# Kernel optimization log

Measured on AMD Instinct MI355X. Metric: run time of the kernel, lower is better.

## Reference

```python
import jax, jax.numpy as jnp
import numpy as np

WIN = 7
K1, K2 = 0.01, 0.03
NP_ = WIN * WIN
COV_NORM = NP_ / (NP_ - 1)


def _box_conv(x, w):
    return jax.lax.conv_general_dilated(
        x, w, window_strides=(1, 1), padding='VALID',
        dimension_numbers=('NCHW', 'OIHW', 'NCHW'))


def setup_inputs() -> dict:
    key = jax.random.key(0)
    k1, k2 = jax.random.split(key)
    B, C, H, W = 64, 2, 320, 320
    X = jax.random.uniform(k1, (B, C, H, W), dtype=jnp.float32)
    Y = jax.random.uniform(k2, (B, C, H, W), dtype=jnp.float32)
    data_range = jnp.ones((B, 1, 1, 1), dtype=jnp.float32)
    w = jnp.ones((1, C, WIN, WIN), dtype=jnp.float32) / (WIN * WIN)
    return {"X": X, "Y": Y, "data_range": data_range, "w": w}


def reference(X, Y, data_range, w):
    C1 = (K1 * data_range) ** 2
    C2 = (K2 * data_range) ** 2
    ux = _box_conv(X, w)
    uy = _box_conv(Y, w)
    uxx = _box_conv(X * X, w)
    uyy = _box_conv(Y * Y, w)
    uxy = _box_conv(X * Y, w)
    vx = COV_NORM * (uxx - ux * ux)
    vy = COV_NORM * (uyy - uy * uy)
    vxy = COV_NORM * (uxy - ux * uy)
    A1 = 2 * ux * uy + C1
    A2 = 2 * vxy + C2
    B1 = ux ** 2 + uy ** 2 + C1
    B2 = vx + vy + C2
    S = (A1 * A2) / (B1 * B2)
    return 1 - S.mean()
```

## Files before the change

kernel.cpp:

```cpp
#include <hip/hip_runtime.h>

#define WW 320
#define OWID 314
#define OHEI 314
#define BB 64
#define CW 58
#define NCW 6
#define BROWS 40
#define NBAND 8
#define BPB 2
#define WPB (NCW * BPB)
#define NTH (WPB * 64)
#define NBLK (BB * NBAND / BPB)

#define LOADR(K_)                                                             \
  {                                                                           \
    const int rr  = min(r0 + g7 + (K_), WW - 1);      \
    const int off = rr * WW;                         \
    gx0[K_] = X0[off]; gx1[K_] = X1[off];                                     \
    gy0[K_] = Y0[off]; gy1[K_] = Y1[off];                                     \
  }

#define BODY(K_)                                                              \
  {                                                                           \
    const float x0 = gx0[K_], x1 = gx1[K_];                                   \
    const float y0 = gy0[K_], y1 = gy1[K_];                                   \
    const float px  = x0 + x1;                                                \
    const float py  = y0 + y1;                                                \
    const float p2  = x0 * x0 + x1 * x1 + y0 * y0 + y1 * y1;                  \
    const float pxy = x0 * y0 + x1 * y1;                                      \
    V0 += px  - ring[K_][0]; ring[K_][0] = px;                                \
    V1 += py  - ring[K_][1]; ring[K_][1] = py;                                \
    V2 += p2  - ring[K_][2]; ring[K_][2] = p2;                                \
    V3 += pxy - ring[K_][3]; ring[K_][3] = pxy;                               \
    const int i_ = g7 + (K_);                                                 \
    const int t  = r0 + i_ - 6;                               \
    if (i_ >= 6 && t < tmax) {                         \
      float b0 = V0 + __shfl_down(V0, 1, 64);                                 \
      float b1 = V1 + __shfl_down(V1, 1, 64);                                 \
      float b2 = V2 + __shfl_down(V2, 1, 64);                                 \
      float b3 = V3 + __shfl_down(V3, 1, 64);                                 \
      float q0 = b0 + __shfl_down(b0, 2, 64);                                 \
      float q1 = b1 + __shfl_down(b1, 2, 64);                                 \
      float q2 = b2 + __shfl_down(b2, 2, 64);                                 \
      float q3 = b3 + __shfl_down(b3, 2, 64);                                 \
      float H0 = q0 + __shfl_down(b0, 4, 64) + __shfl_down(V0, 6, 64);        \
      float H1 = q1 + __shfl_down(b1, 4, 64) + __shfl_down(V1, 6, 64);        \
      float H2 = q2 + __shfl_down(b2, 4, 64) + __shfl_down(V2, 6, 64);        \
      float H3 = q3 + __shfl_down(b3, 4, 64) + __shfl_down(V3, 6, 64);        \
      const float ux  = H0 * inv, uy = H1 * inv;                              \
      const float u2  = H2 * inv, uxy = H3 * inv;                             \
      const float vxy = cn * (uxy - ux * uy);                                 \
      const float v2m = cn * (u2 - ux * ux - uy * uy);           \
      const float A1  = 2.0f * ux * uy + C1;                                  \
      const float A2  = 2.0f * vxy + C2;                                      \
      const float B1  = ux * ux + uy * uy + C1;                               \
      const float B2  = v2m + C2;                                             \
      ssum += cmf * (A1 * A2) / (B1 * B2);         \
    }                                                                         \
  }

__global__ __launch_bounds__(NTH, 1) void ssim_main(
    const float* __restrict__ X, const float* __restrict__ Y,
    const float* __restrict__ dr, double* __restrict__ acc,
    unsigned* __restrict__ counter, float* __restrict__ out)
{
    const int w    = threadIdx.x >> 6;
    const int lane = threadIdx.x & 63;
    const int b    = blockIdx.x >> 2;
    const int pair = blockIdx.x & 3;
    const int band = pair * BPB + (w / NCW);
    const int r0   = band * BROWS;
    const int tmax = min(r0 + BROWS, OHEI);

    int c = (w % NCW) * CW + lane;
    const float cmf = (lane < CW && c < OWID) ? 1.0f : 0.0f;
    if (c > WW - 1) c = WW - 1;

    const size_t plane = (size_t)WW * WW;
    const float* X0 = X + (size_t)b * 2 * plane + c;
    const float* X1 = X0 + plane;
    const float* Y0 = Y + (size_t)b * 2 * plane + c;
    const float* Y1 = Y0 + plane;

    const float d  = dr[b];
    const float C1 = (0.01f * d) * (0.01f * d);
    const float C2 = (0.03f * d) * (0.03f * d);
    const float inv = 1.0f / 49.0f;
    const float cn  = 49.0f / 48.0f;

    float ring[7][4];
    #pragma unroll
    for (int k = 0; k < 7; ++k) {
        ring[k][0] = 0.0f; ring[k][1] = 0.0f;
        ring[k][2] = 0.0f; ring[k][3] = 0.0f;
    }
    float V0 = 0.0f, V1 = 0.0f, V2 = 0.0f, V3 = 0.0f;
    float ssum = 0.0f;
    float gx0[7], gx1[7], gy0[7], gy1[7];

    #pragma unroll 1
    for (int g7 = 0; g7 < 49; g7 += 7) {
        LOADR(0) LOADR(1) LOADR(2) LOADR(3) LOADR(4) LOADR(5) LOADR(6)
        BODY(0) BODY(1) BODY(2) BODY(3) BODY(4) BODY(5) BODY(6)
    }

    double local = (double)ssum;
    #pragma unroll
    for (int off = 32; off > 0; off >>= 1)
        local += __shfl_down(local, off, 64);
    __shared__ double wsum[WPB];
    if (lane == 0) wsum[w] = local;
    __syncthreads();
    if (threadIdx.x == 0) {
        double tot = 0.0;
        #pragma unroll
        for (int k = 0; k < WPB; ++k) tot += wsum[k];
        atomicAdd(acc, tot);
        __threadfence();
        unsigned ticket = atomicAdd(counter, 1u);
        if (ticket == NBLK - 1) {
            double stot = atomicAdd(acc, 0.0);
            const double N = (double)BB * (double)OHEI * (double)OWID;
            out[0] = (float)(1.0 - stot / N);
        }
    }
}

extern "C" void kernel_launch(void* const* d_in, const int* in_sizes, int n_in,
                              void* d_out, int out_size, void* d_ws, size_t ws_size,
                              hipStream_t stream)
{
    const float* X  = (const float*)d_in[0];
    const float* Y  = (const float*)d_in[1];
    const float* dr = (const float*)d_in[2];
    double*   acc     = (double*)d_ws;
    unsigned* counter = (unsigned*)((char*)d_ws + 8);
    float*    out     = (float*)d_out;

    hipMemsetAsync(d_ws, 0, 16, stream);
    ssim_main<<<dim3(NBLK), dim3(NTH), 0, stream>>>(X, Y, dr, acc, counter, out);
}
```

Baseline: 136.7 us.

## Process two columns per lane with float2 loads and shorter row bands

Each lane now handles two adjacent output columns, loaded with float2, and shares partial horizontal sums between the even and odd columns through a paired shuffle scheme. That cuts the column overlap between waves from 6 waves of 58 columns to 3 waves of 122 columns. Row bands shrink from 40 to 20, giving 16 bands per image in 4 blocks of 12 waves each. The aim is fewer redundant loads and fewer shuffles per output. The costs are more vertical halo rows per output and more registers for the doubled ring buffer.

```diff
diff --git a/kernel.cpp b/kernel.cpp
--- a/kernel.cpp
+++ b/kernel.cpp
@@ -4,59 +4,81 @@
 #define OWID 314
 #define OHEI 314
 #define BB 64
-#define CW 58
-#define NCW 6
-#define BROWS 40
-#define NBAND 8
-#define BPB 2
-#define WPB (NCW * BPB)
+#define CPW 122
+#define NCW 3
+#define BROWS 20
+#define NBANDB 4
+#define WPB (NCW * NBANDB)
 #define NTH (WPB * 64)
-#define NBLK (BB * NBAND / BPB)
+#define NBLK (BB * 4)
 
 #define LOADR(K_)                                                             \
   {                                                                           \
     const int rr  = min(r0 + g7 + (K_), WW - 1);      \
-    const int off = rr * WW;                         \
-    gx0[K_] = X0[off]; gx1[K_] = X1[off];                                     \
-    gy0[K_] = Y0[off]; gy1[K_] = Y1[off];                                     \
+    const int off = rr * WW;                                \
+    gx0[K_] = *(const float2*)(X0p + off);                                    \
+    gx1[K_] = *(const float2*)(X1p + off);                                    \
+    gy0[K_] = *(const float2*)(Y0p + off);                                    \
+    gy1[K_] = *(const float2*)(Y1p + off);                                    \
+  }
+
+#define HPAIR(VE, VO, HE, HO)                                                 \
+  {                                                                           \
+    const float P  = (VE) + (VO);                                             \
+    const float t1 = P + __shfl_down(P, 1, 64);                               \
+    const float T  = t1 + __shfl_down(P, 2, 64);                              \
+    HE = T + __shfl_down((VE), 3, 64);                                        \
+    HO = T - (VE) + __shfl_down(P, 3, 64);                                    \
   }
 
 #define BODY(K_)                                                              \
   {                                                                           \
-    const float x0 = gx0[K_], x1 = gx1[K_];                                   \
-    const float y0 = gy0[K_], y1 = gy1[K_];                                   \
-    const float px  = x0 + x1;                                                \
-    const float py  = y0 + y1;                                                \
-    const float p2  = x0 * x0 + x1 * x1 + y0 * y0 + y1 * y1;                  \
-    const float pxy = x0 * y0 + x1 * y1;                                      \
-    V0 += px  - ring[K_][0]; ring[K_][0] = px;                                \
-    V1 += py  - ring[K_][1]; ring[K_][1] = py;                                \
-    V2 += p2  - ring[K_][2]; ring[K_][2] = p2;                                \
-    V3 += pxy - ring[K_][3]; ring[K_][3] = pxy;                               \
+    const float2 x0 = gx0[K_], x1 = gx1[K_];                                  \
+    const float2 y0 = gy0[K_], y1 = gy1[K_];                                  \
+    const float pxe  = x0.x + x1.x,  pxo  = x0.y + x1.y;                      \
+    const float pye  = y0.x + y1.x,  pyo  = y0.y + y1.y;                      \
+    const float p2e  = x0.x * x0.x + x1.x * x1.x + y0.x * y0.x + y1.x * y1.x; \
+    const float p2o  = x0.y * x0.y + x1.y * x1.y + y0.y * y0.y + y1.y * y1.y; \
+    const float pxye = x0.x * y0.x + x1.x * y1.x;                             \
+    const float pxyo = x0.y * y0.y + x1.y * y1.y;                             \
+    V0e += pxe  - ring[K_][0]; ring[K_][0] = pxe;                             \
+    V0o += pxo  - ring[K_][1]; ring[K_][1] = pxo;                             \
+    V1e += pye  - ring[K_][2]; ring[K_][2] = pye;                             \
+    V1o += pyo  - ring[K_][3]; ring[K_][3] = pyo;                             \
+    V2e += p2e  - ring[K_][4]; ring[K_][4] = p2e;                             \
+    V2o += p2o  - ring[K_][5]; ring[K_][5] = p2o;                             \
+    V3e += pxye - ring[K_][6]; ring[K_][6] = pxye;                            \
+    V3o += pxyo - ring[K_][7]; ring[K_][7] = pxyo;                            \
     const int i_ = g7 + (K_);                                                 \
     const int t  = r0 + i_ - 6;                               \
     if (i_ >= 6 && t < tmax) {                         \
-      float b0 = V0 + __shfl_down(V0, 1, 64);                                 \
-      float b1 = V1 + __shfl_down(V1, 1, 64);                                 \
-      float b2 = V2 + __shfl_down(V2, 1, 64);                                 \
-      float b3 = V3 + __shfl_down(V3, 1, 64);                                 \
-      float q0 = b0 + __shfl_down(b0, 2, 64);                                 \
-      float q1 = b1 + __shfl_down(b1, 2, 64);                                 \
-      float q2 = b2 + __shfl_down(b2, 2, 64);                                 \
-      float q3 = b3 + __shfl_down(b3, 2, 64);                                 \
-      float H0 = q0 + __shfl_down(b0, 4, 64) + __shfl_down(V0, 6, 64);        \
-      float H1 = q1 + __shfl_down(b1, 4, 64) + __shfl_down(V1, 6, 64);        \
-      float H2 = q2 + __shfl_down(b2, 4, 64) + __shfl_down(V2, 6, 64);        \
-      float H3 = q3 + __shfl_down(b3, 4, 64) + __shfl_down(V3, 6, 64);        \
-      const float ux  = H0 * inv, uy = H1 * inv;                              \
-      const float u2  = H2 * inv, uxy = H3 * inv;                             \
-      const float vxy = cn * (uxy - ux * uy);                                 \
-      const float v2m = cn * (u2 - ux * ux - uy * uy);           \
-      const float A1  = 2.0f * ux * uy + C1;                                  \
-      const float A2  = 2.0f * vxy + C2;                                      \
-      const float B1  = ux * ux + uy * uy + C1;                               \
-      const float B2  = v2m + C2;                                             \
-      ssum += cmf * (A1 * A2) / (B1 * B2);         \
+      float H0e, H0o, H1e, H1o, H2e, H2o, H3e, H3o;                           \
+      HPAIR(V0e, V0o, H0e, H0o)                                               \
+      HPAIR(V1e, V1o, H1e, H1o)                                               \
+      HPAIR(V2e, V2o, H2e, H2o)                                               \
+      HPAIR(V3e, V3o, H3e, H3o)                                               \
+      {                                                                       \
+        const float ux = H0e * inv, uy = H1e * inv;                           \
+        const float u2 = H2e * inv, uxy = H3e * inv;                          \
+        const float vxy = cn * (uxy - ux * uy);                               \
+        const float v2m = cn * (u2 - ux * ux - uy * uy);                      \
+        const float A1 = 2.0f * ux * uy + C1;                                 \
+        const float A2 = 2.0f * vxy + C2;                                     \
+        const float B1 = ux * ux + uy * uy + C1;                              \
+        const float B2 = v2m + C2;                                            \
+        ssum += cmf0 * (A1 * A2) / (B1 * B2);                                 \
+      }                                                                       \
+      {                                                                       \
+        const float ux = H0o * inv, uy = H1o * inv;                           \
+        const float u2 = H2o * inv, uxy = H3o * inv;                          \
+        const float vxy = cn * (uxy - ux * uy);                               \
+        const float v2m = cn * (u2 - ux * ux - uy * uy);                      \
+        const float A1 = 2.0f * ux * uy + C1;                                 \
+        const float A2 = 2.0f * vxy + C2;                                     \
+        const float B1 = ux * ux + uy * uy + C1;                              \
+        const float B2 = v2m + C2;                                            \
+        ssum += cmf1 * (A1 * A2) / (B1 * B2);                                 \
+      }                                                                       \
     }                                                                         \
   }
 
@@ -68,20 +90,22 @@
     const int w    = threadIdx.x >> 6;
     const int lane = threadIdx.x & 63;
     const int b    = blockIdx.x >> 2;
-    const int pair = blockIdx.x & 3;
-    const int band = pair * BPB + (w / NCW);
+    const int q    = blockIdx.x & 3;
+    const int band = q * NBANDB + (w / NCW);
     const int r0   = band * BROWS;
     const int tmax = min(r0 + BROWS, OHEI);
 
-    int c = (w % NCW) * CW + lane;
-    const float cmf = (lane < CW && c < OWID) ? 1.0f : 0.0f;
-    if (c > WW - 1) c = WW - 1;
+    const int base = (w % NCW) * CPW;
+    int c0 = base + 2 * lane;
+    const float cmf0 = (lane <= 60 && c0     < OWID) ? 1.0f : 0.0f;
+    const float cmf1 = (lane <= 60 && c0 + 1 < OWID) ? 1.0f : 0.0f;
+    if (c0 > WW - 2) c0 = WW - 2;
 
     const size_t plane = (size_t)WW * WW;
-    const float* X0 = X + (size_t)b * 2 * plane + c;
-    const float* X1 = X0 + plane;
-    const float* Y0 = Y + (size_t)b * 2 * plane + c;
-    const float* Y1 = Y0 + plane;
+    const float* X0p = X + (size_t)b * 2 * plane + c0;
+    const float* X1p = X0p + plane;
+    const float* Y0p = Y + (size_t)b * 2 * plane + c0;
+    const float* Y1p = Y0p + plane;
 
     const float d  = dr[b];
     const float C1 = (0.01f * d) * (0.01f * d);
@@ -89,18 +113,19 @@
     const float inv = 1.0f / 49.0f;
     const float cn  = 49.0f / 48.0f;
 
-    float ring[7][4];
+    float ring[7][8];
     #pragma unroll
-    for (int k = 0; k < 7; ++k) {
-        ring[k][0] = 0.0f; ring[k][1] = 0.0f;
-        ring[k][2] = 0.0f; ring[k][3] = 0.0f;
-    }
-    float V0 = 0.0f, V1 = 0.0f, V2 = 0.0f, V3 = 0.0f;
+    for (int k = 0; k < 7; ++k)
+        #pragma unroll
+        for (int m = 0; m < 8; ++m) ring[k][m] = 0.0f;
+
+    float V0e = 0.0f, V0o = 0.0f, V1e = 0.0f, V1o = 0.0f;
+    float V2e = 0.0f, V2o = 0.0f, V3e = 0.0f, V3o = 0.0f;
     float ssum = 0.0f;
-    float gx0[7], gx1[7], gy0[7], gy1[7];
+    float2 gx0[7], gx1[7], gy0[7], gy1[7];
 
     #pragma unroll 1
-    for (int g7 = 0; g7 < 49; g7 += 7) {
+    for (int g7 = 0; g7 < 28; g7 += 7) {
         LOADR(0) LOADR(1) LOADR(2) LOADR(3) LOADR(4) LOADR(5) LOADR(6)
         BODY(0) BODY(1) BODY(2) BODY(3) BODY(4) BODY(5) BODY(6)
     }
```

Result: slower. 146.8 us (+7.4%).
